# Kernel tuning notes

Measured on AMD Instinct MI355X. Metric: run time of the kernel, lower is better.

## Reference

```python
import jax, jax.numpy as jnp
import numpy as np

B, N, D, E, FF, TOP_K = 4, 1024, 1024, 8, 4096, 2

def setup_inputs() -> dict:
    key = jax.random.key(0)
    ks = jax.random.split(key, 6)
    s = lambda k, shape: (jax.random.normal(k, shape, jnp.float32) * 0.02)
    x  = jax.random.normal(ks[0], (B, N, D), jnp.float32)
    Wr = s(ks[1], (E, D))            # router: logits = x @ Wr.T (no bias)
    W1 = s(ks[2], (E, D, FF)); b1 = jnp.zeros((E, FF), jnp.float32)  # fc1
    Wg = s(ks[3], (E, D, FF)); bg = jnp.zeros((E, FF), jnp.float32)  # fc_gate
    W2 = s(ks[4], (E, FF, D)); b2 = jnp.zeros((E, D), jnp.float32)   # fc2
    return {"x": x, "Wr": Wr, "W1": W1, "b1": b1, "Wg": Wg, "bg": bg, "W2": W2, "b2": b2}

def reference(x, Wr, W1, b1, Wg, bg, W2, b2):
    Bb, Nn, Dd = x.shape
    xf = x.reshape(-1, Dd)                      # [T, D]
    T = xf.shape[0]
    logits = xf @ Wr.T                          # [T, E]
    probs = jax.nn.softmax(logits, axis=-1)
    topv, topi = jax.lax.top_k(probs, TOP_K)    # [T, K]
    topv = topv / (topv.sum(-1, keepdims=True) + 1e-6)
    # per-(expert,token) combine weight: comb[t, e] = sum_k topv[t,k] * (topi[t,k]==e)
    comb = jnp.zeros((T, E), x.dtype).at[jnp.arange(T)[:, None], topi].add(topv)
    # scan over experts (fixed small E) to keep memory to one [T, FF] at a time
    def step(acc, p):
        w1, bb1, wg, bbg, w2, bb2, we = p       # we: [T]
        h = xf @ w1 + bb1                       # [T, FF]
        g = xf @ wg + bbg
        out = (jax.nn.silu(g) * h) @ w2 + bb2   # [T, D]
        return acc + we[:, None] * out, None
    acc, _ = jax.lax.scan(step, jnp.zeros((T, Dd), x.dtype), (W1, b1, Wg, bg, W2, b2, comb.T))
    out_final = acc.reshape(Bb, Nn, Dd)
    # load-balance aux loss (computed under no_grad in torch)
    counts = jnp.zeros((E,), x.dtype).at[topi.reshape(-1)].add(1.0)
    frac = counts / (counts.sum() + 1e-6)
    lb = jax.lax.stop_gradient((frac * probs.sum(0)).sum() * E)
    return out_final, lb
```

## Files before the change

kernel.cpp:

```cpp
#include <hip/hip_runtime.h>
#include <hip/hip_bf16.h>
#include <math.h>

#define T_TOK 4096
#define D_DIM 1024
#define E_EXP 8
#define FF_DIM 4096
#define NROWS (T_TOK * 2)
#define MAXT1 40
#define MAXT2 72

typedef unsigned short u16;
typedef unsigned int u32;
typedef __attribute__((ext_vector_type(8))) short bf16x8;
typedef __attribute__((ext_vector_type(4))) float f32x4;
typedef __attribute__((ext_vector_type(2))) unsigned int u32x2;
typedef __attribute__((ext_vector_type(4))) short s16x4;

__device__ __forceinline__ u16 f2bf(float f) {
    union { float f; unsigned u; } v; v.f = f;
    unsigned r = v.u + 0x7FFFu + ((v.u >> 16) & 1u);
    return (u16)(r >> 16);
}

typedef const __attribute__((address_space(1))) u32* gas1_t;
typedef __attribute__((address_space(3))) u32* las3_t;
#define GLOAD16(g, l) __builtin_amdgcn_global_load_lds((gas1_t)(const void*)(g), (las3_t)(void*)(l), 16, 0, 0)
#define MFMA(a, b, c) __builtin_amdgcn_mfma_f32_16x16x32_bf16((a), (b), (c), 0, 0, 0)
#define CVTPK(dst, lo, hi) asm("v_cvt_pk_bf16_f32 %0, %1, %2" : "=v"(dst) : "v"(lo), "v"(hi))
#define CFENCE() asm volatile("" ::: "memory")
#define SIGB(r) (((r) ^ ((r) >> 2)) & 7)


__global__ void k_init(int* cnt, float* probsum) {
    int i = threadIdx.x;
    if (i < E_EXP) { cnt[i] = 0; probsum[i] = 0.f; }
}

__global__ __launch_bounds__(256) void k_router(
    const float* __restrict__ x, const float* __restrict__ Wr,
    int* __restrict__ tok_e, float* __restrict__ tok_w,
    int* __restrict__ cnt, float* __restrict__ probsum)
{
    __shared__ float bp[E_EXP];
    __shared__ int   bc[E_EXP];
    const int tid = threadIdx.x;
    if (tid < E_EXP) { bp[tid] = 0.f; bc[tid] = 0; }
    __syncthreads();
    const int wave = tid >> 6, lane = tid & 63;
    const int t = blockIdx.x * 4 + wave;
    const float* xt = x + (size_t)t * D_DIM;
    float a[E_EXP] = {0.f,0.f,0.f,0.f,0.f,0.f,0.f,0.f};
    for (int j = lane; j < D_DIM; j += 64) {
        float xv = xt[j];
        #pragma unroll
        for (int e = 0; e < E_EXP; e++) a[e] = fmaf(xv, Wr[e * D_DIM + j], a[e]);
    }
    #pragma unroll
    for (int e = 0; e < E_EXP; e++) {
        #pragma unroll
        for (int off = 32; off; off >>= 1) a[e] += __shfl_xor(a[e], off, 64);
    }
    if (lane == 0) {
        float mx = a[0];
        #pragma unroll
        for (int e = 1; e < E_EXP; e++) mx = fmaxf(mx, a[e]);
        float p[E_EXP], s = 0.f;
        #pragma unroll
        for (int e = 0; e < E_EXP; e++) { p[e] = expf(a[e] - mx); s += p[e]; }
        float inv = 1.f / s;
        #pragma unroll
        for (int e = 0; e < E_EXP; e++) { p[e] *= inv; atomicAdd(&bp[e], p[e]); }
        int e0 = 0; float v0 = p[0];
        #pragma unroll
        for (int e = 1; e < E_EXP; e++) if (p[e] > v0) { v0 = p[e]; e0 = e; }
        int e1 = -1; float v1 = -1.f;
        #pragma unroll
        for (int e = 0; e < E_EXP; e++) if (e != e0 && p[e] > v1) { v1 = p[e]; e1 = e; }
        float sv = v0 + v1 + 1e-6f;
        tok_e[2*t] = e0; tok_e[2*t+1] = e1;
        tok_w[2*t] = v0 / sv; tok_w[2*t+1] = v1 / sv;
        atomicAdd(&bc[e0], 1); atomicAdd(&bc[e1], 1);
    }
    __syncthreads();
    if (tid < E_EXP) { atomicAdd(&cnt[tid], bc[tid]); atomicAdd(&probsum[tid], bp[tid]); }
}

__global__ void k_prefix(const int* __restrict__ cnt, const float* __restrict__ probsum,
                         int* __restrict__ basep, int* __restrict__ cursor,
                         float* __restrict__ out_lb,
                         int* __restrict__ nt1, int* __restrict__ te1, int* __restrict__ tm1,
                         int* __restrict__ nt2, int* __restrict__ te2, int* __restrict__ tm2)
{
    if (threadIdx.x == 0) {
        int b = 0; float lb = 0.f;
        for (int e = 0; e < E_EXP; e++) {
            basep[e] = b; b += cnt[e];
            lb += ((float)cnt[e] / (8192.f + 1e-6f)) * probsum[e];
        }
        *out_lb = lb * (float)E_EXP;
        int n1 = 0, n2 = 0;
        for (int e = 0; e < E_EXP; e++) {
            for (int m = 0; m < cnt[e]; m += 256) { te1[n1] = e; tm1[n1] = m; n1++; }
            for (int m = 0; m < cnt[e]; m += 128) { te2[n2] = e; tm2[n2] = m; n2++; }
        }
        *nt1 = n1; *nt2 = n2;
    }
    if (threadIdx.x < E_EXP) cursor[threadIdx.x] = 0;
}

__global__ void k_assign(const int* __restrict__ tok_e, const float* __restrict__ tok_w,
                         const int* __restrict__ basep, int* __restrict__ cursor,
                         int* __restrict__ row_token, int* __restrict__ row_slot,
                         float* __restrict__ row_weight)
{
    int t = blockIdx.x * blockDim.x + threadIdx.x;
    if (t >= T_TOK) return;
    #pragma unroll
    for (int k = 0; k < 2; k++) {
        int e = tok_e[2*t + k];
        int pos = basep[e] + atomicAdd(&cursor[e], 1);
        row_token[pos] = t; row_slot[pos] = k; row_weight[pos] = tok_w[2*t + k];
    }
}

__global__ __launch_bounds__(256) void k_cvt_x(const float* __restrict__ in, u16* __restrict__ out) {
    size_t i = ((size_t)blockIdx.x * 256 + threadIdx.x) * 8;
    f32x4 a = *(const f32x4*)(in + i);
    f32x4 b = *(const f32x4*)(in + i + 4);
    bf16x8 o;
    #pragma unroll
    for (int j = 0; j < 4; j++) { o[j] = (short)f2bf(a[j]); o[j + 4] = (short)f2bf(b[j]); }
    *(bf16x8*)(out + i) = o;
}

__global__ __launch_bounds__(256) void k_cvt_w2(const float* __restrict__ W2, u16* __restrict__ w2t) {
    __shared__ u16 t[64][68];
    const float* in = W2 + (size_t)blockIdx.z * FF_DIM * D_DIM;
    u16* out = w2t + (size_t)blockIdx.z * FF_DIM * D_DIM;
    const int R = FF_DIM, C = D_DIM;
    const int r0 = blockIdx.y * 64, c0 = blockIdx.x * 64;
    const int tid = threadIdx.x;
    const int lr = tid >> 4, lc = (tid & 15) * 4;
    #pragma unroll
    for (int i = 0; i < 4; i++) {
        const int r = lr + i * 16;
        f32x4 v = *(const f32x4*)(in + (size_t)(r0 + r) * C + c0 + lc);
        s16x4 w;
        #pragma unroll
        for (int j = 0; j < 4; j++) w[j] = (short)f2bf(v[j]);
        *(s16x4*)&t[r][lc] = w;
    }
    __syncthreads();
    #pragma unroll
    for (int i = 0; i < 4; i++) {
        const int c = lr + i * 16;
        s16x4 w;
        #pragma unroll
        for (int j = 0; j < 4; j++) w[j] = (short)t[lc + j][c];
        *(s16x4*)(out + (size_t)(c0 + c) * R + r0 + lc) = w;
    }
}


__global__ __launch_bounds__(512, 2) void k_pass1(
    const u16* __restrict__ xbf,
    const float* __restrict__ W1, const float* __restrict__ Wg,
    const float* __restrict__ b1v, const float* __restrict__ bgv,
    const int* __restrict__ cnt, const int* __restrict__ basep,
    const int* __restrict__ row_token,
    const int* __restrict__ ntp, const int* __restrict__ te, const int* __restrict__ tm,
    u16* __restrict__ hg)
{
    const int ty = blockIdx.y;
    if (ty >= *ntp) return;
    const int e = te[ty];
    const int m0 = tm[ty];
    const int count = cnt[e];
    const int rbase = basep[e];
    const int n0 = blockIdx.x * 128;

    __shared__ __align__(16) u16 LDS[2 * 32768];

    const int tid = threadIdx.x;
    const int l = tid & 63;
    const int w = tid >> 6;

    const int rb = tid >> 3;
    const int swA = ((tid & 7) ^ ((tid >> 3) & 7)) * 8;
    const u16* sA[4];
    #pragma unroll
    for (int s = 0; s < 4; s++) {
        int g = m0 + rb + s * 64; if (g > count - 1) g = count - 1;
        sA[s] = xbf + (size_t)row_token[rbase + g] * D_DIM + swA;
    }

    const int nq = tid & 31;
    const int kq = tid >> 5;
    const float* pBh = W1 + ((size_t)e * D_DIM + kq * 4) * FF_DIM + n0 + nq * 4;
    const float* pBg = Wg + ((size_t)e * D_DIM + kq * 4) * FF_DIM + n0 + nq * 4;
    const int cW = kq >> 1;
    const int offW = (kq & 1) * 4;
    int wdst[4];
    #pragma unroll
    for (int j = 0; j < 4; j++) {
        const int row = nq * 4 + j;
        wdst[j] = row * 64 + (cW ^ SIGB(row)) * 8 + offW;
    }

    const int wm = w >> 2, wn = w & 3;
    const int fr = l & 15, q = l >> 4;
    const int s7 = fr & 7;

    f32x4 acc_h[8][2], acc_g[8][2];
    const f32x4 z4 = {0.f, 0.f, 0.f, 0.f};
    #pragma unroll
    for (int mf = 0; mf < 8; mf++)
        #pragma unroll
        for (int nf = 0; nf < 2; nf++) { acc_h[mf][nf] = z4; acc_g[mf][nf] = z4; }

    f32x4 vb0, vb1, vb2, vb3;

    #define LOADB1(P, K0) do { \
        const float* p_ = (P) + (size_t)(K0) * FF_DIM; \
        vb0 = *(const f32x4*)(p_); \
        vb1 = *(const f32x4*)(p_ + FF_DIM); \
        vb2 = *(const f32x4*)(p_ + 2 * FF_DIM); \
        vb3 = *(const f32x4*)(p_ + 3 * FF_DIM); \
    } while (0)

    #define CVTW1(BASE) do { \
        _Pragma("unroll") \
        for (int j = 0; j < 4; j++) { \
            u32 lo_, hi_; u32x2 wv_; \
            CVTPK(lo_, vb0[j], vb1[j]); \
            CVTPK(hi_, vb2[j], vb3[j]); \
            wv_.x = lo_; wv_.y = hi_; \
            *(u32x2*)&LDS[(BASE) + wdst[j]] = wv_; \
        } \
    } while (0)

    #define STAGE_A1(B, K0) do { \
        _Pragma("unroll") \
        for (int s = 0; s < 4; s++) \
            GLOAD16(sA[s] + (K0), &LDS[(B) * 32768 + s * 4096 + tid * 8]); \
    } while (0)

    auto COMP = [&](int kk, int ab) {
        const int rsA = ((kk * 4 + q) ^ s7) * 8;
        const int rB0 = wn * 32 + fr, rB1 = wn * 32 + 16 + fr;
        const int cb0 = ((kk * 4 + q) ^ SIGB(rB0)) * 8;
        const int cb1 = ((kk * 4 + q) ^ SIGB(rB1)) * 8;
        bf16x8 bh0 = *(const bf16x8*)&LDS[ab + 16384 + rB0 * 64 + cb0];
        bf16x8 bg0 = *(const bf16x8*)&LDS[ab + 24576 + rB0 * 64 + cb0];
        bf16x8 bh1 = *(const bf16x8*)&LDS[ab + 16384 + rB1 * 64 + cb1];
        bf16x8 bg1 = *(const bf16x8*)&LDS[ab + 24576 + rB1 * 64 + cb1];
        #define LDA1(i) (*(const bf16x8*)&LDS[ab + (wm * 128 + (i) * 16 + fr) * 64 + rsA])
        #define MF4(areg, i) do { \
            __builtin_amdgcn_s_setprio(1); \
            acc_h[i][0] = MFMA(areg, bh0, acc_h[i][0]); \
            acc_h[i][1] = MFMA(areg, bh1, acc_h[i][1]); \
            acc_g[i][0] = MFMA(areg, bg0, acc_g[i][0]); \
            acc_g[i][1] = MFMA(areg, bg1, acc_g[i][1]); \
            __builtin_amdgcn_s_setprio(0); } while (0)
        bf16x8 aA = LDA1(0);
        bf16x8 aB = LDA1(1);
        bf16x8 aC;
        aC = LDA1(2); MF4(aA, 0);
        aA = LDA1(3); MF4(aB, 1);
        aB = LDA1(4); MF4(aC, 2);
        aC = LDA1(5); MF4(aA, 3);
        aA = LDA1(6); MF4(aB, 4);
        aB = LDA1(7); MF4(aC, 5);
        MF4(aA, 6);
        MF4(aB, 7);
        #undef LDA1
        #undef MF4
    };

    const int NT = D_DIM / 64;
    LOADB1(pBh, 0);
    CVTW1(0 + 16384);
    STAGE_A1(0, 0);
    LOADB1(pBg, 0);
    CVTW1(0 + 24576);
    asm volatile("s_waitcnt vmcnt(0) lgkmcnt(0)" ::: "memory");
    __builtin_amdgcn_s_barrier();
    CFENCE();

    int b = 0;
    #pragma unroll 1
    for (int t = 0; t < NT; ++t) {
        const int ab = b * 32768;
        const int nboff = (b ^ 1) * 32768;
        const int kN = (t + 1 < NT ? t + 1 : NT - 1) * 64;
        LOADB1(pBh, kN);
        COMP(0, ab);
        CVTW1(nboff + 16384);
        STAGE_A1(b ^ 1, kN);
        LOADB1(pBg, kN);
        COMP(1, ab);
        CVTW1(nboff + 24576);
        asm volatile("s_waitcnt vmcnt(0) lgkmcnt(0)" ::: "memory");
        __builtin_amdgcn_s_barrier();
        CFENCE();
        b ^= 1;
    }
    asm volatile("s_waitcnt vmcnt(0)" ::: "memory");
    #undef LOADB1
    #undef CVTW1
    #undef STAGE_A1

    const float* b1p = b1v + (size_t)e * FF_DIM + n0;
    const float* bgp = bgv + (size_t)e * FF_DIM + n0;
    #pragma unroll
    for (int mf = 0; mf < 8; mf++) {
        const int rl = wm * 128 + mf * 16 + q * 4;
        #pragma unroll
        for (int r = 0; r < 4; r++) {
            const int g = m0 + rl + r;
            if (g < count) {
                u16* orow = hg + (size_t)(rbase + g) * FF_DIM + n0;
                #pragma unroll
                for (int nf = 0; nf < 2; nf++) {
                    const int col = wn * 32 + nf * 16 + fr;
                    float hv = acc_h[mf][nf][r] + b1p[col];
                    float gv = acc_g[mf][nf][r] + bgp[col];
                    float sig = 1.f / (1.f + expf(-gv));
                    orow[col] = f2bf(gv * sig * hv);
                }
            }
        }
    }
}


__global__ __launch_bounds__(256, 2) void k_pass2(
    const u16* __restrict__ hg,
    const u16* __restrict__ w2t, const float* __restrict__ b2v,
    const int* __restrict__ cnt, const int* __restrict__ basep,
    const int* __restrict__ row_token, const int* __restrict__ row_slot,
    const float* __restrict__ row_weight,
    const int* __restrict__ ntp, const int* __restrict__ te, const int* __restrict__ tm,
    float* __restrict__ contrib)
{
    const int ty = blockIdx.y;
    if (ty >= *ntp) return;
    const int e = te[ty];
    const int m0 = tm[ty];
    const int count = cnt[e];
    const int rbase = basep[e];
    const int n0 = blockIdx.x * 128;

    __shared__ __align__(16) u16 LDS[2 * 16384];

    const int tid = threadIdx.x;
    const int l = tid & 63;
    const int w = tid >> 6;

    const int rb = tid >> 3;
    const int sw0 = ((tid & 7) ^ ((tid >> 3) & 7)) * 8;
    const u16* sA[4];
    #pragma unroll
    for (int s = 0; s < 4; s++) {
        int g = m0 + rb + s * 32; if (g > count - 1) g = count - 1;
        sA[s] = hg + (size_t)(rbase + g) * FF_DIM + sw0;
    }
    const u16* sB[4];
    #pragma unroll
    for (int s = 0; s < 4; s++)
        sB[s] = w2t + ((size_t)e * D_DIM + (size_t)(n0 + rb + s * 32)) * FF_DIM + sw0;

    const int wm = w >> 1, wn = w & 1;
    const int fr = l & 15, q = l >> 4;
    const int s7 = fr & 7;

    f32x4 acc[4][4];
    const f32x4 z4 = {0.f, 0.f, 0.f, 0.f};
    #pragma unroll
    for (int mf = 0; mf < 4; mf++)
        #pragma unroll
        for (int nf = 0; nf < 4; nf++) acc[mf][nf] = z4;

    auto STAGE = [&](int b, int k0) {
        #pragma unroll
        for (int s = 0; s < 4; s++)
            GLOAD16(sA[s] + k0, &LDS[b * 16384 + s * 2048 + tid * 8]);
        #pragma unroll
        for (int s = 0; s < 4; s++)
            GLOAD16(sB[s] + k0, &LDS[b * 16384 + 8192 + s * 2048 + tid * 8]);
    };

    const int NT = FF_DIM / 64;
    STAGE(0, 0);
    int cur = 0;
    #pragma unroll 1
    for (int t = 0; t < NT; ++t) {
        if (t + 1 < NT) {
            STAGE(cur ^ 1, (t + 1) * 64);
            asm volatile("s_waitcnt vmcnt(8)" ::: "memory");
        } else {
            asm volatile("s_waitcnt vmcnt(0)" ::: "memory");
        }
        __builtin_amdgcn_s_barrier();
        CFENCE();
        const int ab = cur * 16384;
        #pragma unroll
        for (int kk = 0; kk < 2; kk++) {
            const int rs = ((kk * 4 + q) ^ s7) * 8;
            bf16x8 a[4], bb[4];
            #pragma unroll
            for (int mf = 0; mf < 4; mf++)
                a[mf] = *(const bf16x8*)&LDS[ab + (wm * 64 + mf * 16 + fr) * 64 + rs];
            #pragma unroll
            for (int nf = 0; nf < 4; nf++)
                bb[nf] = *(const bf16x8*)&LDS[ab + 8192 + (wn * 64 + nf * 16 + fr) * 64 + rs];
            __builtin_amdgcn_s_setprio(1);
            #pragma unroll
            for (int mf = 0; mf < 4; mf++)
                #pragma unroll
                for (int nf = 0; nf < 4; nf++)
                    acc[mf][nf] = MFMA(a[mf], bb[nf], acc[mf][nf]);
            __builtin_amdgcn_s_setprio(0);
        }
        CFENCE();
        __builtin_amdgcn_s_barrier();
        cur ^= 1;
    }

    const float* b2p = b2v + (size_t)e * D_DIM + n0;
    #pragma unroll
    for (int mf = 0; mf < 4; mf++) {
        const int rl = wm * 64 + mf * 16 + q * 4;
        #pragma unroll
        for (int r = 0; r < 4; r++) {
            const int g = m0 + rl + r;
            if (g < count) {
                const int token = row_token[rbase + g];
                const int slot  = row_slot[rbase + g];
                const float wgt_ = row_weight[rbase + g];
                float* orow = contrib + ((size_t)slot * T_TOK + token) * D_DIM + n0;
                #pragma unroll
                for (int nf = 0; nf < 4; nf++) {
                    const int col = wn * 64 + nf * 16 + fr;
                    orow[col] = wgt_ * (acc[mf][nf][r] + b2p[col]);
                }
            }
        }
    }
}

__global__ void k_combine(const float* __restrict__ contrib, float* __restrict__ out) {
    int i = blockIdx.x * blockDim.x + threadIdx.x;
    const f32x4* c0 = (const f32x4*)contrib;
    const f32x4* c1 = c0 + ((size_t)T_TOK * D_DIM / 4);
    f32x4* o = (f32x4*)out;
    o[i] = c0[i] + c1[i];
}


extern "C" void kernel_launch(void* const* d_in, const int* in_sizes, int n_in,
                              void* d_out, int out_size, void* d_ws, size_t ws_size,
                              hipStream_t stream)
{
    (void)in_sizes; (void)n_in; (void)out_size; (void)ws_size;
    const float* x  = (const float*)d_in[0];
    const float* Wr = (const float*)d_in[1];
    const float* W1 = (const float*)d_in[2];
    const float* b1 = (const float*)d_in[3];
    const float* Wg = (const float*)d_in[4];
    const float* bg = (const float*)d_in[5];
    const float* W2 = (const float*)d_in[6];
    const float* b2 = (const float*)d_in[7];
    float* out = (float*)d_out;

    char* ws = (char*)d_ws;
    u16* xbf = (u16*)ws;             ws += (size_t)T_TOK * D_DIM * sizeof(u16);
    u16* w2t = (u16*)ws;             ws += (size_t)E_EXP * D_DIM * FF_DIM * sizeof(u16);
    u16* hg = (u16*)ws;              ws += (size_t)NROWS * FF_DIM * sizeof(u16);
    float* contrib = (float*)ws;     ws += (size_t)2 * T_TOK * D_DIM * sizeof(float);
    int* tok_e = (int*)ws;           ws += (size_t)T_TOK * 2 * sizeof(int);
    float* tok_w = (float*)ws;       ws += (size_t)T_TOK * 2 * sizeof(float);
    int* row_token = (int*)ws;       ws += (size_t)NROWS * sizeof(int);
    int* row_slot = (int*)ws;        ws += (size_t)NROWS * sizeof(int);
    float* row_weight = (float*)ws;  ws += (size_t)NROWS * sizeof(float);
    int* cnt = (int*)ws;             ws += 8 * sizeof(int);
    int* basep = (int*)ws;           ws += 8 * sizeof(int);
    int* cursor = (int*)ws;          ws += 8 * sizeof(int);
    float* probsum = (float*)ws;     ws += 8 * sizeof(float);
    int* nt1 = (int*)ws;             ws += sizeof(int);
    int* nt2 = (int*)ws;             ws += sizeof(int);
    int* te1 = (int*)ws;             ws += MAXT1 * sizeof(int);
    int* tm1 = (int*)ws;             ws += MAXT1 * sizeof(int);
    int* te2 = (int*)ws;             ws += MAXT2 * sizeof(int);
    int* tm2 = (int*)ws;             ws += MAXT2 * sizeof(int);

    k_init<<<1, 64, 0, stream>>>(cnt, probsum);
    k_cvt_x<<<(T_TOK * D_DIM / 8) / 256, 256, 0, stream>>>(x, xbf);
    k_cvt_w2<<<dim3(D_DIM / 64, FF_DIM / 64, E_EXP), 256, 0, stream>>>(W2, w2t);
    k_router<<<T_TOK / 4, 256, 0, stream>>>(x, Wr, tok_e, tok_w, cnt, probsum);
    k_prefix<<<1, 64, 0, stream>>>(cnt, probsum, basep, cursor, out + (size_t)T_TOK * D_DIM,
                                   nt1, te1, tm1, nt2, te2, tm2);
    k_assign<<<T_TOK / 256, 256, 0, stream>>>(tok_e, tok_w, basep, cursor, row_token, row_slot, row_weight);
    k_pass1<<<dim3(FF_DIM / 128, MAXT1), 512, 0, stream>>>(xbf, W1, Wg, b1, bg, cnt, basep, row_token,
                                                           nt1, te1, tm1, hg);
    k_pass2<<<dim3(D_DIM / 128, MAXT2), 256, 0, stream>>>(hg, w2t, b2, cnt, basep, row_token, row_slot, row_weight,
                                                          nt2, te2, tm2, contrib);
    k_combine<<<(T_TOK * D_DIM / 4) / 256, 256, 0, stream>>>(contrib, out);
}
```

Baseline: 467.2 us.

## Fold W2 bf16 transpose-convert into pass1 blocks, drop separate kernel

Removes the standalone W2 convert/transpose kernel and moves that work into k_pass1. Each pass1 block runs a grid-stride loop over the W2 64x64 tiles after its GEMM work, so blocks that exit early (ty >= ntp) and the tail of the grid fill idle time with conversion. It saves one kernel launch and overlaps the bandwidth-bound conversion with compute-bound pass1 work. The cost is extra memory traffic competing with the pass1 GEMM, and a longer runtime for every pass1 block, even the busy ones.

```diff
diff --git a/kernel.cpp b/kernel.cpp
--- a/kernel.cpp
+++ b/kernel.cpp
@@ -9,6 +9,8 @@
 #define NROWS (T_TOK * 2)
 #define MAXT1 40
 #define MAXT2 72
+#define NBLK1 (32 * MAXT1)
+#define W2TILES (E_EXP * (FF_DIM / 64) * (D_DIM / 64))
 
 typedef unsigned short u16;
 typedef unsigned int u32;
@@ -134,201 +136,210 @@
     *(bf16x8*)(out + i) = o;
 }
 
-__global__ __launch_bounds__(256) void k_cvt_w2(const float* __restrict__ W2, u16* __restrict__ w2t) {
-    __shared__ u16 t[64][68];
-    const float* in = W2 + (size_t)blockIdx.z * FF_DIM * D_DIM;
-    u16* out = w2t + (size_t)blockIdx.z * FF_DIM * D_DIM;
-    const int R = FF_DIM, C = D_DIM;
-    const int r0 = blockIdx.y * 64, c0 = blockIdx.x * 64;
-    const int tid = threadIdx.x;
-    const int lr = tid >> 4, lc = (tid & 15) * 4;
-    #pragma unroll
-    for (int i = 0; i < 4; i++) {
-        const int r = lr + i * 16;
-        f32x4 v = *(const f32x4*)(in + (size_t)(r0 + r) * C + c0 + lc);
-        s16x4 w;
-        #pragma unroll
-        for (int j = 0; j < 4; j++) w[j] = (short)f2bf(v[j]);
-        *(s16x4*)&t[r][lc] = w;
-    }
-    __syncthreads();
-    #pragma unroll
-    for (int i = 0; i < 4; i++) {
-        const int c = lr + i * 16;
-        s16x4 w;
-        #pragma unroll
-        for (int j = 0; j < 4; j++) w[j] = (short)t[lc + j][c];
-        *(s16x4*)(out + (size_t)(c0 + c) * R + r0 + lc) = w;
-    }
-}
-
 
 __global__ __launch_bounds__(512, 2) void k_pass1(
     const u16* __restrict__ xbf,
     const float* __restrict__ W1, const float* __restrict__ Wg,
     const float* __restrict__ b1v, const float* __restrict__ bgv,
+    const float* __restrict__ W2, u16* __restrict__ w2t,
     const int* __restrict__ cnt, const int* __restrict__ basep,
     const int* __restrict__ row_token,
     const int* __restrict__ ntp, const int* __restrict__ te, const int* __restrict__ tm,
     u16* __restrict__ hg)
 {
+    __shared__ __align__(16) u16 LDS[2 * 32768];
+    const int tid = threadIdx.x;
     const int ty = blockIdx.y;
-    if (ty >= *ntp) return;
-    const int e = te[ty];
-    const int m0 = tm[ty];
-    const int count = cnt[e];
-    const int rbase = basep[e];
-    const int n0 = blockIdx.x * 128;
-
-    __shared__ __align__(16) u16 LDS[2 * 32768];
-
-    const int tid = threadIdx.x;
-    const int l = tid & 63;
-    const int w = tid >> 6;
-
-    const int rb = tid >> 3;
-    const int swA = ((tid & 7) ^ ((tid >> 3) & 7)) * 8;
-    const u16* sA[4];
-    #pragma unroll
-    for (int s = 0; s < 4; s++) {
-        int g = m0 + rb + s * 64; if (g > count - 1) g = count - 1;
-        sA[s] = xbf + (size_t)row_token[rbase + g] * D_DIM + swA;
-    }
-
-    const int nq = tid & 31;
-    const int kq = tid >> 5;
-    const float* pBh = W1 + ((size_t)e * D_DIM + kq * 4) * FF_DIM + n0 + nq * 4;
-    const float* pBg = Wg + ((size_t)e * D_DIM + kq * 4) * FF_DIM + n0 + nq * 4;
-    const int cW = kq >> 1;
-    const int offW = (kq & 1) * 4;
-    int wdst[4];
-    #pragma unroll
-    for (int j = 0; j < 4; j++) {
-        const int row = nq * 4 + j;
-        wdst[j] = row * 64 + (cW ^ SIGB(row)) * 8 + offW;
-    }
-
-    const int wm = w >> 2, wn = w & 3;
-    const int fr = l & 15, q = l >> 4;
-    const int s7 = fr & 7;
-
-    f32x4 acc_h[8][2], acc_g[8][2];
-    const f32x4 z4 = {0.f, 0.f, 0.f, 0.f};
-    #pragma unroll
-    for (int mf = 0; mf < 8; mf++)
-        #pragma unroll
-        for (int nf = 0; nf < 2; nf++) { acc_h[mf][nf] = z4; acc_g[mf][nf] = z4; }
-
-    f32x4 vb0, vb1, vb2, vb3;
-
-    #define LOADB1(P, K0) do { \
-        const float* p_ = (P) + (size_t)(K0) * FF_DIM; \
-        vb0 = *(const f32x4*)(p_); \
-        vb1 = *(const f32x4*)(p_ + FF_DIM); \
-        vb2 = *(const f32x4*)(p_ + 2 * FF_DIM); \
-        vb3 = *(const f32x4*)(p_ + 3 * FF_DIM); \
-    } while (0)
-
-    #define CVTW1(BASE) do { \
-        _Pragma("unroll") \
-        for (int j = 0; j < 4; j++) { \
-            u32 lo_, hi_; u32x2 wv_; \
-            CVTPK(lo_, vb0[j], vb1[j]); \
-            CVTPK(hi_, vb2[j], vb3[j]); \
-            wv_.x = lo_; wv_.y = hi_; \
-            *(u32x2*)&LDS[(BASE) + wdst[j]] = wv_; \
-        } \
-    } while (0)
-
-    #define STAGE_A1(B, K0) do { \
-        _Pragma("unroll") \
-        for (int s = 0; s < 4; s++) \
-            GLOAD16(sA[s] + (K0), &LDS[(B) * 32768 + s * 4096 + tid * 8]); \
-    } while (0)
-
-    auto COMP = [&](int kk, int ab) {
-        const int rsA = ((kk * 4 + q) ^ s7) * 8;
-        const int rB0 = wn * 32 + fr, rB1 = wn * 32 + 16 + fr;
-        const int cb0 = ((kk * 4 + q) ^ SIGB(rB0)) * 8;
-        const int cb1 = ((kk * 4 + q) ^ SIGB(rB1)) * 8;
-        bf16x8 bh0 = *(const bf16x8*)&LDS[ab + 16384 + rB0 * 64 + cb0];
-        bf16x8 bg0 = *(const bf16x8*)&LDS[ab + 24576 + rB0 * 64 + cb0];
-        bf16x8 bh1 = *(const bf16x8*)&LDS[ab + 16384 + rB1 * 64 + cb1];
-        bf16x8 bg1 = *(const bf16x8*)&LDS[ab + 24576 + rB1 * 64 + cb1];
-        #define LDA1(i) (*(const bf16x8*)&LDS[ab + (wm * 128 + (i) * 16 + fr) * 64 + rsA])
-        #define MF4(areg, i) do { \
-            __builtin_amdgcn_s_setprio(1); \
-            acc_h[i][0] = MFMA(areg, bh0, acc_h[i][0]); \
-            acc_h[i][1] = MFMA(areg, bh1, acc_h[i][1]); \
-            acc_g[i][0] = MFMA(areg, bg0, acc_g[i][0]); \
-            acc_g[i][1] = MFMA(areg, bg1, acc_g[i][1]); \
-            __builtin_amdgcn_s_setprio(0); } while (0)
-        bf16x8 aA = LDA1(0);
-        bf16x8 aB = LDA1(1);
-        bf16x8 aC;
-        aC = LDA1(2); MF4(aA, 0);
-        aA = LDA1(3); MF4(aB, 1);
-        aB = LDA1(4); MF4(aC, 2);
-        aC = LDA1(5); MF4(aA, 3);
-        aA = LDA1(6); MF4(aB, 4);
-        aB = LDA1(7); MF4(aC, 5);
-        MF4(aA, 6);
-        MF4(aB, 7);
-        #undef LDA1
-        #undef MF4
-    };
-
-    const int NT = D_DIM / 64;
-    LOADB1(pBh, 0);
-    CVTW1(0 + 16384);
-    STAGE_A1(0, 0);
-    LOADB1(pBg, 0);
-    CVTW1(0 + 24576);
-    asm volatile("s_waitcnt vmcnt(0) lgkmcnt(0)" ::: "memory");
-    __builtin_amdgcn_s_barrier();
-    CFENCE();
-
-    int b = 0;
-    #pragma unroll 1
-    for (int t = 0; t < NT; ++t) {
-        const int ab = b * 32768;
-        const int nboff = (b ^ 1) * 32768;
-        const int kN = (t + 1 < NT ? t + 1 : NT - 1) * 64;
-        LOADB1(pBh, kN);
-        COMP(0, ab);
-        CVTW1(nboff + 16384);
-        STAGE_A1(b ^ 1, kN);
-        LOADB1(pBg, kN);
-        COMP(1, ab);
-        CVTW1(nboff + 24576);
+
+    if (ty < *ntp) {
+        const int e = te[ty];
+        const int m0 = tm[ty];
+        const int count = cnt[e];
+        const int rbase = basep[e];
+        const int n0 = blockIdx.x * 128;
+
+        const int l = tid & 63;
+        const int w = tid >> 6;
+
+        const int rb = tid >> 3;
+        const int swA = ((tid & 7) ^ ((tid >> 3) & 7)) * 8;
+        const u16* sA[4];
+        #pragma unroll
+        for (int s = 0; s < 4; s++) {
+            int g = m0 + rb + s * 64; if (g > count - 1) g = count - 1;
+            sA[s] = xbf + (size_t)row_token[rbase + g] * D_DIM + swA;
+        }
+
+        const int nq = tid & 31;
+        const int kq = tid >> 5;
+        const float* pBh = W1 + ((size_t)e * D_DIM + kq * 4) * FF_DIM + n0 + nq * 4;
+        const float* pBg = Wg + ((size_t)e * D_DIM + kq * 4) * FF_DIM + n0 + nq * 4;
+        const int cW = kq >> 1;
+        const int offW = (kq & 1) * 4;
+        int wdst[4];
+        #pragma unroll
+        for (int j = 0; j < 4; j++) {
+            const int row = nq * 4 + j;
+            wdst[j] = row * 64 + (cW ^ SIGB(row)) * 8 + offW;
+        }
+
+        const int wm = w >> 2, wn = w & 3;
+        const int fr = l & 15, q = l >> 4;
+        const int s7 = fr & 7;
+
+        f32x4 acc_h[8][2], acc_g[8][2];
+        const f32x4 z4 = {0.f, 0.f, 0.f, 0.f};
+        #pragma unroll
+        for (int mf = 0; mf < 8; mf++)
+            #pragma unroll
+            for (int nf = 0; nf < 2; nf++) { acc_h[mf][nf] = z4; acc_g[mf][nf] = z4; }
+
+        f32x4 vb0, vb1, vb2, vb3;
+
+        #define LOADB1(P, K0) do { \
+            const float* p_ = (P) + (size_t)(K0) * FF_DIM; \
+            vb0 = *(const f32x4*)(p_); \
+            vb1 = *(const f32x4*)(p_ + FF_DIM); \
+            vb2 = *(const f32x4*)(p_ + 2 * FF_DIM); \
+            vb3 = *(const f32x4*)(p_ + 3 * FF_DIM); \
+        } while (0)
+
+        #define CVTW1(BASE) do { \
+            _Pragma("unroll") \
+            for (int j = 0; j < 4; j++) { \
+                u32 lo_, hi_; u32x2 wv_; \
+                CVTPK(lo_, vb0[j], vb1[j]); \
+                CVTPK(hi_, vb2[j], vb3[j]); \
+                wv_.x = lo_; wv_.y = hi_; \
+                *(u32x2*)&LDS[(BASE) + wdst[j]] = wv_; \
+            } \
+        } while (0)
+
+        #define STAGE_A1(B, K0) do { \
+            _Pragma("unroll") \
+            for (int s = 0; s < 4; s++) \
+                GLOAD16(sA[s] + (K0), &LDS[(B) * 32768 + s * 4096 + tid * 8]); \
+        } while (0)
+
+        auto COMP = [&](int kk, int ab) {
+            const int rsA = ((kk * 4 + q) ^ s7) * 8;
+            const int rB0 = wn * 32 + fr, rB1 = wn * 32 + 16 + fr;
+            const int cb0 = ((kk * 4 + q) ^ SIGB(rB0)) * 8;
+            const int cb1 = ((kk * 4 + q) ^ SIGB(rB1)) * 8;
+            bf16x8 bh0 = *(const bf16x8*)&LDS[ab + 16384 + rB0 * 64 + cb0];
+            bf16x8 bg0 = *(const bf16x8*)&LDS[ab + 24576 + rB0 * 64 + cb0];
+            bf16x8 bh1 = *(const bf16x8*)&LDS[ab + 16384 + rB1 * 64 + cb1];
+            bf16x8 bg1 = *(const bf16x8*)&LDS[ab + 24576 + rB1 * 64 + cb1];
+            #define LDA1(i) (*(const bf16x8*)&LDS[ab + (wm * 128 + (i) * 16 + fr) * 64 + rsA])
+            #define MF4(areg, i) do { \
+                __builtin_amdgcn_s_setprio(1); \
+                acc_h[i][0] = MFMA(areg, bh0, acc_h[i][0]); \
+                acc_h[i][1] = MFMA(areg, bh1, acc_h[i][1]); \
+                acc_g[i][0] = MFMA(areg, bg0, acc_g[i][0]); \
+                acc_g[i][1] = MFMA(areg, bg1, acc_g[i][1]); \
+                __builtin_amdgcn_s_setprio(0); } while (0)
+            bf16x8 aA = LDA1(0);
+            bf16x8 aB = LDA1(1);
+            bf16x8 aC;
+            aC = LDA1(2); MF4(aA, 0);
+            aA = LDA1(3); MF4(aB, 1);
+            aB = LDA1(4); MF4(aC, 2);
+            aC = LDA1(5); MF4(aA, 3);
+            aA = LDA1(6); MF4(aB, 4);
+            aB = LDA1(7); MF4(aC, 5);
+            MF4(aA, 6);
+            MF4(aB, 7);
+            #undef LDA1
+            #undef MF4
+        };
+
+        const int NT = D_DIM / 64;
+        LOADB1(pBh, 0);
+        CVTW1(0 + 16384);
+        STAGE_A1(0, 0);
+        LOADB1(pBg, 0);
+        CVTW1(0 + 24576);
         asm volatile("s_waitcnt vmcnt(0) lgkmcnt(0)" ::: "memory");
         __builtin_amdgcn_s_barrier();
         CFENCE();
-        b ^= 1;
-    }
-    asm volatile("s_waitcnt vmcnt(0)" ::: "memory");
-    #undef LOADB1
-    #undef CVTW1
-    #undef STAGE_A1
-
-    const float* b1p = b1v + (size_t)e * FF_DIM + n0;
-    const float* bgp = bgv + (size_t)e * FF_DIM + n0;
-    #pragma unroll
-    for (int mf = 0; mf < 8; mf++) {
-        const int rl = wm * 128 + mf * 16 + q * 4;
-        #pragma unroll
-        for (int r = 0; r < 4; r++) {
-            const int g = m0 + rl + r;
-            if (g < count) {
-                u16* orow = hg + (size_t)(rbase + g) * FF_DIM + n0;
+
+        int b = 0;
+        #pragma unroll 1
+        for (int t = 0; t < NT; ++t) {
+            const int ab = b * 32768;
+            const int nboff = (b ^ 1) * 32768;
+            const int kN = (t + 1 < NT ? t + 1 : NT - 1) * 64;
+            LOADB1(pBh, kN);
+            COMP(0, ab);
+            CVTW1(nboff + 16384);
+            STAGE_A1(b ^ 1, kN);
+            LOADB1(pBg, kN);
+            COMP(1, ab);
+            CVTW1(nboff + 24576);
+            asm volatile("s_waitcnt vmcnt(0) lgkmcnt(0)" ::: "memory");
+            __builtin_amdgcn_s_barrier();
+            CFENCE();
+            b ^= 1;
+        }
+        asm volatile("s_waitcnt vmcnt(0)" ::: "memory");
+        #undef LOADB1
+        #undef CVTW1
+        #undef STAGE_A1
+
+        const float* b1p = b1v + (size_t)e * FF_DIM + n0;
+        const float* bgp = bgv + (size_t)e * FF_DIM + n0;
+        #pragma unroll
+        for (int mf = 0; mf < 8; mf++) {
+            const int rl = wm * 128 + mf * 16 + q * 4;
+            #pragma unroll
+            for (int r = 0; r < 4; r++) {
+                const int g = m0 + rl + r;
+                if (g < count) {
+                    u16* orow = hg + (size_t)(rbase + g) * FF_DIM + n0;
+                    #pragma unroll
+                    for (int nf = 0; nf < 2; nf++) {
+                        const int col = wn * 32 + nf * 16 + fr;
+                        float hv = acc_h[mf][nf][r] + b1p[col];
+                        float gv = acc_g[mf][nf][r] + bgp[col];
+                        float sig = 1.f / (1.f + expf(-gv));
+                        orow[col] = f2bf(gv * sig * hv);
+                    }
+                }
+            }
+        }
+    }
+
+    {
+        const int bid = ty * gridDim.x + blockIdx.x;
+        const int lr = tid >> 4;
+        const int lc = (tid & 15) * 4;
+        u16* tbuf = LDS;
+        #pragma unroll 1
+        for (int tile = bid; tile < W2TILES; tile += NBLK1) {
+            const int e2 = tile >> 10;
+            const int rem = tile & 1023;
+            const int r0 = (rem >> 4) * 64;
+            const int c0 = (rem & 15) * 64;
+            const float* in = W2 + ((size_t)e2 * FF_DIM + r0) * D_DIM + c0;
+            u16* outp = w2t + ((size_t)e2 * D_DIM + c0) * FF_DIM + r0;
+            __syncthreads();
+            #pragma unroll
+            for (int h = 0; h < 2; h++) {
+                const int r = lr + h * 32;
+                f32x4 v = *(const f32x4*)(in + (size_t)r * D_DIM + lc);
+                s16x4 wv;
                 #pragma unroll
-                for (int nf = 0; nf < 2; nf++) {
-                    const int col = wn * 32 + nf * 16 + fr;
-                    float hv = acc_h[mf][nf][r] + b1p[col];
-                    float gv = acc_g[mf][nf][r] + bgp[col];
-                    float sig = 1.f / (1.f + expf(-gv));
-                    orow[col] = f2bf(gv * sig * hv);
-                }
+                for (int j = 0; j < 4; j++) wv[j] = (short)f2bf(v[j]);
+                *(s16x4*)&tbuf[r * 68 + lc] = wv;
+            }
+            __syncthreads();
+            #pragma unroll
+            for (int h = 0; h < 2; h++) {
+                const int c = lr + h * 32;
+                s16x4 wv;
+                #pragma unroll
+                for (int j = 0; j < 4; j++) wv[j] = (short)tbuf[(lc + j) * 68 + c];
+                *(s16x4*)(outp + (size_t)c * FF_DIM + lc) = wv;
             }
         }
     }
@@ -497,12 +508,11 @@
 
     k_init<<<1, 64, 0, stream>>>(cnt, probsum);
     k_cvt_x<<<(T_TOK * D_DIM / 8) / 256, 256, 0, stream>>>(x, xbf);
-    k_cvt_w2<<<dim3(D_DIM / 64, FF_DIM / 64, E_EXP), 256, 0, stream>>>(W2, w2t);
     k_router<<<T_TOK / 4, 256, 0, stream>>>(x, Wr, tok_e, tok_w, cnt, probsum);
     k_prefix<<<1, 64, 0, stream>>>(cnt, probsum, basep, cursor, out + (size_t)T_TOK * D_DIM,
                                    nt1, te1, tm1, nt2, te2, tm2);
     k_assign<<<T_TOK / 256, 256, 0, stream>>>(tok_e, tok_w, basep, cursor, row_token, row_slot, row_weight);
-    k_pass1<<<dim3(FF_DIM / 128, MAXT1), 512, 0, stream>>>(xbf, W1, Wg, b1, bg, cnt, basep, row_token,
+    k_pass1<<<dim3(FF_DIM / 128, MAXT1), 512, 0, stream>>>(xbf, W1, Wg, b1, bg, W2, w2t, cnt, basep, row_token,
                                                            nt1, te1, tm1, hg);
     k_pass2<<<dim3(D_DIM / 128, MAXT2), 256, 0, stream>>>(hg, w2t, b2, cnt, basep, row_token, row_slot, row_weight,
                                                           nt2, te2, tm2, contrib);
```

New measurement: 471.4 us. Within noise of the previous version (+0.9%).
